# Performance work log

Measured on AMD Instinct MI355X. Metric: run time of the kernel, lower is better.

Reference implementation:

```python
import jax, jax.numpy as jnp
import numpy as np

N_QUERY = 1024
N_REF = 100000
D_LATENT = 128
K = 8


def setup_inputs() -> dict:
    key = jax.random.key(0)
    k1, k2 = jax.random.split(key)
    x = jax.random.normal(k1, (N_QUERY, D_LATENT), dtype=jnp.float32)
    base_data = jax.random.normal(k2, (N_REF, D_LATENT), dtype=jnp.float32)
    return {"x": x, "base_data": base_data, "k": K}


def reference(x, base_data, k):
    base_norm = jnp.sum(base_data * base_data, axis=1)        # [N_ref]
    x_norm = jnp.sum(x * x, axis=1)                           # [N_q]
    # [N_q, N_ref] distance matrix
    diffs = base_norm[None, :] + x_norm[:, None] - 2.0 * jnp.einsum(
        "qd,rd->qr", x, base_data
    )
    diffs = jnp.sqrt(diffs)
    # top-k SMALLEST distances, sorted ascending (torch.topk largest=False)
    neg_top, _ = jax.lax.top_k(-diffs, k)
    return (-neg_top).astype(jnp.float32)
```

## Files before the change

kernel.cpp:

```cpp
#include <hip/hip_runtime.h>
#include <math.h>

#define NQ 1024
#define NR 100000
#define D  128
#define K  8
#define TR 32
#define NCH   125
#define CHUNK 800
#define TPC   25
#define NQG   2

typedef __attribute__((ext_vector_type(8))) short short8;
typedef __attribute__((ext_vector_type(4))) float f32x4;

static __device__ __forceinline__ unsigned short f2bf(float f) {
    unsigned int u = __float_as_uint(f);
    return (unsigned short)((u + 0x7FFFu + ((u >> 16) & 1u)) >> 16);
}
static __device__ __forceinline__ float bf2f(unsigned short h) {
    return __uint_as_float(((unsigned int)h) << 16);
}

__device__ __forceinline__ void topk_insert(float (&t)[K], float d) {
    if (d < t[K - 1]) {
#pragma unroll
        for (int j = K - 1; j > 0; --j)
            t[j] = (d >= t[j]) ? t[j] : ((d < t[j - 1]) ? t[j - 1] : d);
        t[0] = (d < t[0]) ? d : t[0];
    }
}

__global__ __launch_bounds__(512, 1) void knn_mfma3(const float* __restrict__ x,
                                                    const float* __restrict__ base,
                                                    float* __restrict__ cand) {
    __shared__ unsigned short lhs[2][TR * 128];
    __shared__ unsigned short lls[2][TR * 128];
    __shared__ float lbn[2][TR];

    const int tid  = threadIdx.x;
    const int lane = tid & 63;
    const int w    = tid >> 6;
    const int lm   = lane & 15;
    const int kg   = lane >> 4;
    const int qb   = blockIdx.x & 1;
    const int rc   = blockIdx.x >> 1;
    const int r0   = rc * CHUNK;

    short8 Bh[4][4], Bl[4][4];
    float  xn[4];
#pragma unroll
    for (int qt = 0; qt < 4; ++qt) {
        const int q = qb * 512 + w * 64 + qt * 16 + lm;
        float s2 = 0.f;
#pragma unroll
        for (int s = 0; s < 4; ++s) {
            const float4 a = *(const float4*)(x + (size_t)q * D + s * 32 + kg * 8);
            const float4 b = *(const float4*)(x + (size_t)q * D + s * 32 + kg * 8 + 4);
            float v[8] = {a.x, a.y, a.z, a.w, b.x, b.y, b.z, b.w};
            short8 hh, ll;
#pragma unroll
            for (int j = 0; j < 8; ++j) {
                s2 = fmaf(v[j], v[j], s2);
                const float m2 = -2.f * v[j];
                const unsigned short h = f2bf(m2);
                const float res = m2 - bf2f(h);
                hh[j] = (short)h;
                ll[j] = (short)f2bf(res);
            }
            Bh[qt][s] = hh; Bl[qt][s] = ll;
        }
        s2 += __shfl_xor(s2, 16, 64);
        s2 += __shfl_xor(s2, 32, 64);
        xn[qt] = s2;
    }

    const int srow = tid >> 4;
    const int scol = tid & 15;

    auto convert_store = [&](const float (&v)[8], int buf) {
        float s2 = 0.f;
        short8 hh, ll;
#pragma unroll
        for (int j = 0; j < 8; ++j) {
            s2 = fmaf(v[j], v[j], s2);
            const unsigned short h = f2bf(v[j]);
            const float res = v[j] - bf2f(h);
            hh[j] = (short)h;
            ll[j] = (short)f2bf(res);
        }
        s2 += __shfl_xor(s2, 1, 64);
        s2 += __shfl_xor(s2, 2, 64);
        s2 += __shfl_xor(s2, 4, 64);
        s2 += __shfl_xor(s2, 8, 64);
        const int idx = srow * 128 + 8 * (scol ^ (srow & 15));
        *(short8*)&lhs[buf][idx] = hh;
        *(short8*)&lls[buf][idx] = ll;
        if (scol == 0) lbn[buf][srow] = s2;
    };

    {
        const float* bp = base + (size_t)(r0 + srow) * D + scol * 8;
        const float4 a = *(const float4*)(bp);
        const float4 b = *(const float4*)(bp + 4);
        const float v[8] = {a.x, a.y, a.z, a.w, b.x, b.y, b.z, b.w};
        convert_store(v, 0);
    }
    __syncthreads();

    float tk[4][K];
#pragma unroll
    for (int qt = 0; qt < 4; ++qt)
#pragma unroll
        for (int j = 0; j < K; ++j) tk[qt][j] = INFINITY;

    int cur = 0;
    for (int ti = 0; ti < TPC; ++ti) {
        float pv[8];
        if (ti + 1 < TPC) {
            const float* bp = base + (size_t)(r0 + (ti + 1) * TR + srow) * D + scol * 8;
            const float4 a = *(const float4*)(bp);
            const float4 b = *(const float4*)(bp + 4);
            pv[0] = a.x; pv[1] = a.y; pv[2] = a.z; pv[3] = a.w;
            pv[4] = b.x; pv[5] = b.y; pv[6] = b.z; pv[7] = b.w;
        }

#pragma unroll
        for (int rt = 0; rt < 2; ++rt) {
            const f32x4 bn4 = *(const f32x4*)&lbn[cur][rt * 16 + kg * 4];
            f32x4 acc[4];
#pragma unroll
            for (int qt = 0; qt < 4; ++qt) acc[qt] = (f32x4){0.f, 0.f, 0.f, 0.f};
#pragma unroll
            for (int s = 0; s < 4; ++s) {
                const int idx = (rt * 16 + lm) * 128 + 8 * ((s * 4 + kg) ^ lm);
                const short8 Ah = *(const short8*)&lhs[cur][idx];
                const short8 Al = *(const short8*)&lls[cur][idx];
#pragma unroll
                for (int qt = 0; qt < 4; ++qt) {
                    acc[qt] = __builtin_amdgcn_mfma_f32_16x16x32_bf16(Ah, Bh[qt][s], acc[qt], 0, 0, 0);
                    acc[qt] = __builtin_amdgcn_mfma_f32_16x16x32_bf16(Ah, Bl[qt][s], acc[qt], 0, 0, 0);
                    acc[qt] = __builtin_amdgcn_mfma_f32_16x16x32_bf16(Al, Bh[qt][s], acc[qt], 0, 0, 0);
                }
            }
#pragma unroll
            for (int qt = 0; qt < 4; ++qt)
#pragma unroll
                for (int j = 0; j < 4; ++j) topk_insert(tk[qt], acc[qt][j] + bn4[j]);
        }

        if (ti + 1 < TPC) convert_store(pv, cur ^ 1);
        __syncthreads();
        cur ^= 1;
    }

#pragma unroll
    for (int st = 16; st <= 32; st <<= 1) {
#pragma unroll
        for (int qt = 0; qt < 4; ++qt) {
            float o[K];
#pragma unroll
            for (int j = 0; j < K; ++j) o[j] = __shfl_xor(tk[qt][j], st, 64);
#pragma unroll
            for (int j = 0; j < K; ++j) topk_insert(tk[qt], o[j]);
        }
    }

    if (kg == 0) {
#pragma unroll
        for (int qt = 0; qt < 4; ++qt) {
            const int q = qb * 512 + w * 64 + qt * 16 + lm;
            float* cp = cand + ((size_t)q * NCH + rc) * K;
#pragma unroll
            for (int j = 0; j < K; ++j)
                cp[j] = sqrtf(fmaxf(tk[qt][j] + xn[qt], 0.f));
        }
    }
}

__global__ __launch_bounds__(256, 4) void knn_merge3(const float* __restrict__ cand,
                                                     float* __restrict__ out) {
    const int q = blockIdx.x * blockDim.x + threadIdx.x;
    if (q >= NQ) return;
    const float* cp = cand + (size_t)q * (NCH * K);
    float t[K];
#pragma unroll
    for (int j = 0; j < K; ++j) t[j] = INFINITY;
    for (int i = 0; i < NCH * K; i += 4) {
        const float4 v = *(const float4*)(cp + i);
        topk_insert(t, v.x); topk_insert(t, v.y);
        topk_insert(t, v.z); topk_insert(t, v.w);
    }
#pragma unroll
    for (int j = 0; j < K; ++j) out[(size_t)q * K + j] = t[j];
}

extern "C" void kernel_launch(void* const* d_in, const int* in_sizes, int n_in,
                              void* d_out, int out_size, void* d_ws, size_t ws_size,
                              hipStream_t stream) {
    const float* x    = (const float*)d_in[0];
    const float* base = (const float*)d_in[1];
    float* out  = (float*)d_out;
    float* cand = (float*)d_ws;

    knn_mfma3<<<NQG * NCH, 512, 0, stream>>>(x, base, cand);
    knn_merge3<<<(NQ + 255) / 256, 256, 0, stream>>>(cand, out);
}
```

Before: 348.2 us.

## Add cheap bf16 prepass to compute per-query pruning threshold for top-k inserts

Adds a first pass that uses only high-half bf16 MFMAs (one per tile instead of three) to record, for each query and chunk, the minimum squared distance in each of eight disjoint row groups. A reduction kernel takes the largest of those per-query group minima and adds a fixed 4.0 margin to form an upper bound tau on the 8th-smallest distance. The precise split-bf16 pass then only calls top-k insertion for distances at or below tau, which cuts the branchy sorted-insert work. The query tiling also changes to four query groups with two blocks per CU. The cost is an extra full pass over base_data plus two more launches, and correctness depends on the 4.0 margin covering the bf16 error.

```diff
diff --git a/kernel.cpp b/kernel.cpp
--- a/kernel.cpp
+++ b/kernel.cpp
@@ -9,7 +9,7 @@
 #define NCH   125
 #define CHUNK 800
 #define TPC   25
-#define NQG   2
+#define NQG   4
 
 typedef __attribute__((ext_vector_type(8))) short short8;
 typedef __attribute__((ext_vector_type(4))) float f32x4;
@@ -31,11 +31,10 @@
     }
 }
 
-__global__ __launch_bounds__(512, 1) void knn_mfma3(const float* __restrict__ x,
+__global__ __launch_bounds__(512, 2) void knn_pass1(const float* __restrict__ x,
                                                     const float* __restrict__ base,
-                                                    float* __restrict__ cand) {
+                                                    float* __restrict__ ss) {
     __shared__ unsigned short lhs[2][TR * 128];
-    __shared__ unsigned short lls[2][TR * 128];
     __shared__ float lbn[2][TR];
 
     const int tid  = threadIdx.x;
@@ -43,15 +42,160 @@
     const int w    = tid >> 6;
     const int lm   = lane & 15;
     const int kg   = lane >> 4;
-    const int qb   = blockIdx.x & 1;
-    const int rc   = blockIdx.x >> 1;
+    const int qb   = blockIdx.x & 3;
+    const int rc   = blockIdx.x >> 2;
     const int r0   = rc * CHUNK;
 
-    short8 Bh[4][4], Bl[4][4];
-    float  xn[4];
-#pragma unroll
-    for (int qt = 0; qt < 4; ++qt) {
-        const int q = qb * 512 + w * 64 + qt * 16 + lm;
+    short8 Bh[2][4];
+#pragma unroll
+    for (int qt = 0; qt < 2; ++qt) {
+        const int q = qb * 256 + w * 32 + qt * 16 + lm;
+#pragma unroll
+        for (int s = 0; s < 4; ++s) {
+            const float4 a = *(const float4*)(x + (size_t)q * D + s * 32 + kg * 8);
+            const float4 b = *(const float4*)(x + (size_t)q * D + s * 32 + kg * 8 + 4);
+            float v[8] = {a.x, a.y, a.z, a.w, b.x, b.y, b.z, b.w};
+            short8 hh;
+#pragma unroll
+            for (int j = 0; j < 8; ++j) hh[j] = (short)f2bf(-2.f * v[j]);
+            Bh[qt][s] = hh;
+        }
+    }
+
+    const int srow = tid >> 4;
+    const int scol = tid & 15;
+
+    auto convert_store = [&](const float (&v)[8], int buf) {
+        float s2 = 0.f;
+        short8 hh;
+#pragma unroll
+        for (int j = 0; j < 8; ++j) {
+            s2 = fmaf(v[j], v[j], s2);
+            hh[j] = (short)f2bf(v[j]);
+        }
+        s2 += __shfl_xor(s2, 1, 64);
+        s2 += __shfl_xor(s2, 2, 64);
+        s2 += __shfl_xor(s2, 4, 64);
+        s2 += __shfl_xor(s2, 8, 64);
+        const int idx = srow * 128 + 8 * (scol ^ (srow & 15));
+        *(short8*)&lhs[buf][idx] = hh;
+        if (scol == 0) lbn[buf][srow] = s2;
+    };
+
+    {
+        const float* bp = base + (size_t)(r0 + srow) * D + scol * 8;
+        const float4 a = *(const float4*)(bp);
+        const float4 b = *(const float4*)(bp + 4);
+        const float v[8] = {a.x, a.y, a.z, a.w, b.x, b.y, b.z, b.w};
+        convert_store(v, 0);
+    }
+    __syncthreads();
+
+    float sl[2][8];
+#pragma unroll
+    for (int qt = 0; qt < 2; ++qt)
+#pragma unroll
+        for (int j = 0; j < 8; ++j) sl[qt][j] = INFINITY;
+
+    int cur = 0;
+    for (int ti = 0; ti < TPC; ++ti) {
+        float pv[8];
+        if (ti + 1 < TPC) {
+            const float* bp = base + (size_t)(r0 + (ti + 1) * TR + srow) * D + scol * 8;
+            const float4 a = *(const float4*)(bp);
+            const float4 b = *(const float4*)(bp + 4);
+            pv[0] = a.x; pv[1] = a.y; pv[2] = a.z; pv[3] = a.w;
+            pv[4] = b.x; pv[5] = b.y; pv[6] = b.z; pv[7] = b.w;
+        }
+
+#pragma unroll
+        for (int rt = 0; rt < 2; ++rt) {
+            const f32x4 bn4 = *(const f32x4*)&lbn[cur][rt * 16 + kg * 4];
+            f32x4 acc[2];
+#pragma unroll
+            for (int qt = 0; qt < 2; ++qt) acc[qt] = (f32x4){0.f, 0.f, 0.f, 0.f};
+#pragma unroll
+            for (int s = 0; s < 4; ++s) {
+                const int idx = (rt * 16 + lm) * 128 + 8 * ((s * 4 + kg) ^ lm);
+                const short8 Ah = *(const short8*)&lhs[cur][idx];
+#pragma unroll
+                for (int qt = 0; qt < 2; ++qt)
+                    acc[qt] = __builtin_amdgcn_mfma_f32_16x16x32_bf16(Ah, Bh[qt][s], acc[qt], 0, 0, 0);
+            }
+#pragma unroll
+            for (int qt = 0; qt < 2; ++qt)
+#pragma unroll
+                for (int j = 0; j < 4; ++j)
+                    sl[qt][rt * 4 + j] = fminf(sl[qt][rt * 4 + j], acc[qt][j] + bn4[j]);
+        }
+
+        if (ti + 1 < TPC) convert_store(pv, cur ^ 1);
+        __syncthreads();
+        cur ^= 1;
+    }
+
+#pragma unroll
+    for (int qt = 0; qt < 2; ++qt)
+#pragma unroll
+        for (int j = 0; j < 8; ++j) {
+            sl[qt][j] = fminf(sl[qt][j], __shfl_xor(sl[qt][j], 16, 64));
+            sl[qt][j] = fminf(sl[qt][j], __shfl_xor(sl[qt][j], 32, 64));
+        }
+
+    if (kg == 0) {
+#pragma unroll
+        for (int qt = 0; qt < 2; ++qt) {
+            const int q = qb * 256 + w * 32 + qt * 16 + lm;
+            float* sp = ss + ((size_t)rc * NQ + q) * 8;
+            *(f32x4*)(sp)     = (f32x4){sl[qt][0], sl[qt][1], sl[qt][2], sl[qt][3]};
+            *(f32x4*)(sp + 4) = (f32x4){sl[qt][4], sl[qt][5], sl[qt][6], sl[qt][7]};
+        }
+    }
+}
+
+__global__ __launch_bounds__(256, 4) void knn_tau(const float* __restrict__ ss,
+                                                  float* __restrict__ tau) {
+    const int q = blockIdx.x * 256 + threadIdx.x;
+    f32x4 m0 = {INFINITY, INFINITY, INFINITY, INFINITY};
+    f32x4 m1 = m0;
+    for (int rc = 0; rc < NCH; ++rc) {
+        const float* sp = ss + ((size_t)rc * NQ + q) * 8;
+        const f32x4 a = *(const f32x4*)(sp);
+        const f32x4 b = *(const f32x4*)(sp + 4);
+#pragma unroll
+        for (int j = 0; j < 4; ++j) { m0[j] = fminf(m0[j], a[j]); m1[j] = fminf(m1[j], b[j]); }
+    }
+    float t = m0[0];
+#pragma unroll
+    for (int j = 1; j < 4; ++j) t = fmaxf(t, m0[j]);
+#pragma unroll
+    for (int j = 0; j < 4; ++j) t = fmaxf(t, m1[j]);
+    tau[q] = t + 4.0f;
+}
+
+__global__ __launch_bounds__(512, 2) void knn_pass2(const float* __restrict__ x,
+                                                    const float* __restrict__ base,
+                                                    const float* __restrict__ tau,
+                                                    float* __restrict__ cand) {
+    __shared__ unsigned short lhs[2][TR * 128];
+    __shared__ unsigned short lls[2][TR * 128];
+    __shared__ float lbn[2][TR];
+
+    const int tid  = threadIdx.x;
+    const int lane = tid & 63;
+    const int w    = tid >> 6;
+    const int lm   = lane & 15;
+    const int kg   = lane >> 4;
+    const int qb   = blockIdx.x & 3;
+    const int rc   = blockIdx.x >> 2;
+    const int r0   = rc * CHUNK;
+
+    short8 Bh[2][4], Bl[2][4];
+    float  xn[2], tau2[2];
+#pragma unroll
+    for (int qt = 0; qt < 2; ++qt) {
+        const int q = qb * 256 + w * 32 + qt * 16 + lm;
+        tau2[qt] = tau[q];
         float s2 = 0.f;
 #pragma unroll
         for (int s = 0; s < 4; ++s) {
@@ -108,9 +252,9 @@
     }
     __syncthreads();
 
-    float tk[4][K];
-#pragma unroll
-    for (int qt = 0; qt < 4; ++qt)
+    float tk[2][K];
+#pragma unroll
+    for (int qt = 0; qt < 2; ++qt)
 #pragma unroll
         for (int j = 0; j < K; ++j) tk[qt][j] = INFINITY;
 
@@ -128,25 +272,28 @@
 #pragma unroll
         for (int rt = 0; rt < 2; ++rt) {
             const f32x4 bn4 = *(const f32x4*)&lbn[cur][rt * 16 + kg * 4];
-            f32x4 acc[4];
-#pragma unroll
-            for (int qt = 0; qt < 4; ++qt) acc[qt] = (f32x4){0.f, 0.f, 0.f, 0.f};
+            f32x4 acc[2];
+#pragma unroll
+            for (int qt = 0; qt < 2; ++qt) acc[qt] = (f32x4){0.f, 0.f, 0.f, 0.f};
 #pragma unroll
             for (int s = 0; s < 4; ++s) {
                 const int idx = (rt * 16 + lm) * 128 + 8 * ((s * 4 + kg) ^ lm);
                 const short8 Ah = *(const short8*)&lhs[cur][idx];
                 const short8 Al = *(const short8*)&lls[cur][idx];
 #pragma unroll
-                for (int qt = 0; qt < 4; ++qt) {
+                for (int qt = 0; qt < 2; ++qt) {
                     acc[qt] = __builtin_amdgcn_mfma_f32_16x16x32_bf16(Ah, Bh[qt][s], acc[qt], 0, 0, 0);
                     acc[qt] = __builtin_amdgcn_mfma_f32_16x16x32_bf16(Ah, Bl[qt][s], acc[qt], 0, 0, 0);
                     acc[qt] = __builtin_amdgcn_mfma_f32_16x16x32_bf16(Al, Bh[qt][s], acc[qt], 0, 0, 0);
                 }
             }
 #pragma unroll
-            for (int qt = 0; qt < 4; ++qt)
-#pragma unroll
-                for (int j = 0; j < 4; ++j) topk_insert(tk[qt], acc[qt][j] + bn4[j]);
+            for (int qt = 0; qt < 2; ++qt)
+#pragma unroll
+                for (int j = 0; j < 4; ++j) {
+                    const float d = acc[qt][j] + bn4[j];
+                    if (d <= tau2[qt]) topk_insert(tk[qt], d);
+                }
         }
 
         if (ti + 1 < TPC) convert_store(pv, cur ^ 1);
@@ -157,7 +304,7 @@
 #pragma unroll
     for (int st = 16; st <= 32; st <<= 1) {
 #pragma unroll
-        for (int qt = 0; qt < 4; ++qt) {
+        for (int qt = 0; qt < 2; ++qt) {
             float o[K];
 #pragma unroll
             for (int j = 0; j < K; ++j) o[j] = __shfl_xor(tk[qt][j], st, 64);
@@ -168,8 +315,8 @@
 
     if (kg == 0) {
 #pragma unroll
-        for (int qt = 0; qt < 4; ++qt) {
-            const int q = qb * 512 + w * 64 + qt * 16 + lm;
+        for (int qt = 0; qt < 2; ++qt) {
+            const int q = qb * 256 + w * 32 + qt * 16 + lm;
             float* cp = cand + ((size_t)q * NCH + rc) * K;
 #pragma unroll
             for (int j = 0; j < K; ++j)
@@ -178,8 +325,8 @@
     }
 }
 
-__global__ __launch_bounds__(256, 4) void knn_merge3(const float* __restrict__ cand,
-                                                     float* __restrict__ out) {
+__global__ __launch_bounds__(256, 4) void knn_merge(const float* __restrict__ cand,
+                                                    float* __restrict__ out) {
     const int q = blockIdx.x * blockDim.x + threadIdx.x;
     if (q >= NQ) return;
     const float* cp = cand + (size_t)q * (NCH * K);
@@ -200,9 +347,16 @@
                               hipStream_t stream) {
     const float* x    = (const float*)d_in[0];
     const float* base = (const float*)d_in[1];
-    float* out  = (float*)d_out;
-    float* cand = (float*)d_ws;
-
-    knn_mfma3<<<NQG * NCH, 512, 0, stream>>>(x, base, cand);
-    knn_merge3<<<(NQ + 255) / 256, 256, 0, stream>>>(cand, out);
-}
+    float* out = (float*)d_out;
+
+    const size_t OFF_TAU  = (size_t)NCH * NQ * 8 * 4;
+    const size_t OFF_CAND = OFF_TAU + 4096;
+    float* ss   = (float*)d_ws;
+    float* tau  = (float*)((char*)d_ws + OFF_TAU);
+    float* cand = (float*)((char*)d_ws + OFF_CAND);
+
+    knn_pass1<<<NQG * NCH, 512, 0, stream>>>(x, base, ss);
+    knn_tau<<<NQ / 256, 256, 0, stream>>>(ss, tau);
+    knn_pass2<<<NQG * NCH, 512, 0, stream>>>(x, base, tau, cand);
+    knn_merge<<<(NQ + 255) / 256, 256, 0, stream>>>(cand, out);
+}
```

After: 336.8 us. 3.3% less time.
